# Performance work log

Hardware: AMD Instinct MI355X
Metric: run time of the kernel (lower is better)

## Reference

```python
import jax, jax.numpy as jnp
import numpy as np

B, NQ, NK = 4, 384, 384
D_EQUI, D_QINV, D_KVINV = 64, 256, 256
D_MSG, D_FF, D_OUT = 64, 128, 64
IN_FEATS = 2 * D_MSG + D_EQUI  # 192


def setup_inputs() -> dict:
    key = jax.random.key(0)
    ks = jax.random.split(key, 12)
    s = lambda k, shp, fan: jax.random.normal(k, shp, jnp.float32) / np.sqrt(fan)
    return {
        "q_equi": jax.random.normal(ks[0], (B, NQ, 3, D_EQUI), jnp.float32),
        "q_inv": jax.random.normal(ks[1], (B, NQ, D_QINV), jnp.float32),
        "k_equi": jax.random.normal(ks[2], (B, NK, 3, D_EQUI), jnp.float32),
        "k_inv": jax.random.normal(ks[3], (B, NK, D_KVINV), jnp.float32),
        "Wq": s(ks[4], (D_QINV, D_MSG), D_QINV),
        "bq": jnp.zeros((D_MSG,), jnp.float32),
        "Wk": s(ks[5], (D_KVINV, D_MSG), D_KVINV),
        "bk": jnp.zeros((D_MSG,), jnp.float32),
        "W1": s(ks[6], (IN_FEATS, D_FF), IN_FEATS),
        "b1": jnp.zeros((D_FF,), jnp.float32),
        "W2": s(ks[7], (D_FF, D_OUT), D_FF),
        "b2": jnp.zeros((D_OUT,), jnp.float32),
    }


def reference(q_equi, q_inv, k_equi, k_inv, Wq, bq, Wk, bk, W1, b1, W2, b2):
    # dotprods over the 3 spatial coords, per equi-channel: [B, Nq, Nk, d_equi]
    dotprods = jnp.einsum("bqcd,bkcd->bqkd", q_equi, k_equi)
    q_msg = q_inv @ Wq + bq  # [B, Nq, d_msg]
    k_msg = k_inv @ Wk + bk  # [B, Nk, d_msg]
    b, nq, dm = q_msg.shape
    nk = k_msg.shape[1]
    # expand + concat -> [B, Nq, Nk, in_feats]
    feats = jnp.concatenate(
        [
            jnp.broadcast_to(q_msg[:, :, None, :], (b, nq, nk, dm)),
            jnp.broadcast_to(k_msg[:, None, :, :], (b, nq, nk, dm)),
            dotprods,
        ],
        axis=-1,
    )
    h = jax.nn.silu(feats @ W1 + b1)  # [B, Nq, Nk, d_ff]
    return h @ W2 + b2  # [B, Nq, Nk, d_out]
```

## Files before the change

kernel.cpp:

```cpp
#include <hip/hip_runtime.h>
#include <hip/hip_bf16.h>
#include <stdint.h>
#include <stddef.h>

#define NQ 384
#define NK 384

typedef __attribute__((ext_vector_type(4))) float float4_;
typedef __attribute__((ext_vector_type(8))) short short8;
typedef __attribute__((ext_vector_type(2))) unsigned int uint2_;

__device__ __forceinline__ short f2bf(float f) {
  union { float f; uint32_t u; } v; v.f = f;
  uint32_t u = v.u;
  uint32_t r = (u + 0x7fffu + ((u >> 16) & 1u)) >> 16;
  return (short)r;
}

__device__ __forceinline__ unsigned int pk2(float lo, float hi) {
  __hip_bfloat162 r = __float22bfloat162_rn(make_float2(lo, hi));
  union { __hip_bfloat162 b; unsigned int u; } u; u.b = r;
  return u.u;
}

__global__ __launch_bounds__(256) void prep0(
    const float* __restrict__ Wq, const float* __restrict__ Wk,
    const float* __restrict__ W1, const float* __restrict__ b1,
    const float* __restrict__ bq, const float* __restrict__ bk,
    const float* __restrict__ W2,
    float* __restrict__ Wqc, float* __restrict__ Wkc,
    float* __restrict__ c1, float* __restrict__ c2,
    short* __restrict__ W1dfrag, short* __restrict__ W2frag)
{
  int bid = blockIdx.x, t = threadIdx.x;
  if (bid < 32) {
    int side = bid >> 4;
    int r0 = (bid & 15) * 16;
    const float* W = side ? Wk : Wq;
    const float* W1s = W1 + side * 64 * 128;
    float* Wc = side ? Wkc : Wqc;
    __shared__ float sW[16][64];
    for (int j = t; j < 1024; j += 256) sW[j >> 6][j & 63] = W[(r0 + (j >> 6)) * 64 + (j & 63)];
    __syncthreads();
    int c = t & 127, rg = (t >> 7) * 8;
    float acc[8] = {0.f, 0.f, 0.f, 0.f, 0.f, 0.f, 0.f, 0.f};
    for (int k = 0; k < 64; ++k) {
      float wv = W1s[k * 128 + c];
      #pragma unroll
      for (int j = 0; j < 8; ++j) acc[j] += sW[rg + j][k] * wv;
    }
    for (int j = 0; j < 8; ++j) Wc[(r0 + rg + j) * 128 + c] = acc[j];
  } else if (bid == 32) {
    if (t < 256) {
      int c = t & 127, side = t >> 7;
      const float* bias = side ? bk : bq;
      const float* W1s = W1 + side * 64 * 128;
      float acc = side ? 0.f : b1[c];
      for (int k = 0; k < 64; ++k) acc += bias[k] * W1s[k * 128 + c];
      (side ? c2 : c1)[c] = acc;
    }
  } else {
    for (int idx = t; idx < 8192; idx += 256) {
      int fi = idx >> 9;
      int l  = (idx >> 3) & 63;
      int i  = idx & 7;
      { int n = fi >> 1, s = fi & 1;
        int d = s * 32 + ((l >> 4) << 3) + i;
        int f = n * 16 + (l & 15);
        W1dfrag[idx] = f2bf(W1[(128 + d) * 128 + f]); }
      { int n2 = fi >> 2, s2 = fi & 3;
        int k = s2 * 32 + ((l >> 4) << 3) + i;
        int o = n2 * 16 + (l & 15);
        W2frag[idx] = f2bf(W2[k * 64 + o]); }
    }
  }
}

__global__ __launch_bounds__(256) void prep1(
    const float* __restrict__ q_inv, const float* __restrict__ k_inv,
    const float* __restrict__ Wqc, const float* __restrict__ Wkc,
    const float* __restrict__ c1, const float* __restrict__ c2,
    float* __restrict__ A1, float* __restrict__ A2)
{
  int bid = blockIdx.x, t = threadIdx.x;
  int row0 = bid * 8;
  int side = row0 >= 1536;
  int r0 = row0 - side * 1536;
  const float* inv = (side ? k_inv : q_inv) + (size_t)r0 * 256;
  const float* Wc  = side ? Wkc : Wqc;
  const float* cc  = side ? c2 : c1;
  float* A = (side ? A2 : A1) + (size_t)r0 * 128;

  __shared__ float sI[8][256];
  for (int j = t; j < 2048; j += 256) sI[j >> 8][j & 255] = inv[j];
  __syncthreads();

  int c = t & 127, rg = (t >> 7) * 4;
  float acc[4] = {0.f, 0.f, 0.f, 0.f};
  for (int k = 0; k < 256; ++k) {
    float wv = Wc[k * 128 + c];
    #pragma unroll
    for (int j = 0; j < 4; ++j) acc[j] += sI[rg + j][k] * wv;
  }
  float cv = cc[c];
  #pragma unroll
  for (int j = 0; j < 4; ++j) A[(size_t)(rg + j) * 128 + c] = acc[j] + cv;
}

__global__ __launch_bounds__(512) void main_kernel(
    const float* __restrict__ q_equi, const float* __restrict__ k_equi,
    const float* __restrict__ A1, const float* __restrict__ A2,
    const short* __restrict__ W1dfrag, const short* __restrict__ W2frag,
    const float* __restrict__ b2, float* __restrict__ out)
{
  int bid = blockIdx.x;
  int b = bid / 576;
  int rem = bid - b * 576;
  int tq = rem / 24, tk = rem - (rem / 24) * 24;
  int q0 = tq * 16, k0 = tk * 16;

  __shared__ __align__(16) char smem[32768];
  float* sK = (float*)smem;

  int tid = threadIdx.x;
  int w = tid >> 6, l = tid & 63;
  int g = l >> 4, r16 = l & 15;

  const float* ksrc = k_equi + ((size_t)(b * NK + k0)) * 192;
  {
    int u = tid;
    int r = u / 48, jj = u - r * 48;
    int j = jj ^ (r & 7);
    __builtin_amdgcn_global_load_lds(ksrc + r * 192 + j * 4, smem + u * 16, 16, 0, 0);
    if (tid < 256) {
      int u2 = tid + 512;
      int r2 = u2 / 48, jj2 = u2 - r2 * 48;
      int j2 = jj2 ^ (r2 & 7);
      __builtin_amdgcn_global_load_lds(ksrc + r2 * 192 + j2 * 4, smem + u2 * 16, 16, 0, 0);
    }
  }
  __syncthreads();

  const float* qrow0 = q_equi + ((size_t)(b * NQ + q0 + 2 * w)) * 192;
  const float* krow = sK + r16 * 48 * 4;
  int x7 = r16 & 7;
  short8 afrag[2][2];
  #pragma unroll
  for (int s = 0; s < 2; ++s) {
    int d0 = s * 32 + g * 8;
    float4_ kva[3], kvb[3];
    #pragma unroll
    for (int c = 0; c < 3; ++c) {
      int j0 = c * 16 + s * 8 + g * 2;
      kva[c] = *(const float4_*)&krow[((j0) ^ x7) * 4];
      kvb[c] = *(const float4_*)&krow[((j0 + 1) ^ x7) * 4];
    }
    #pragma unroll
    for (int m = 0; m < 2; ++m) {
      const float* qrow = qrow0 + m * 192;
      float da[4] = {0.f, 0.f, 0.f, 0.f};
      float db[4] = {0.f, 0.f, 0.f, 0.f};
      #pragma unroll
      for (int c = 0; c < 3; ++c) {
        float4_ qva = *(const float4_*)&qrow[c * 64 + d0];
        float4_ qvb = *(const float4_*)&qrow[c * 64 + d0 + 4];
        #pragma unroll
        for (int i = 0; i < 4; ++i) {
          da[i] += qva[i] * kva[c][i];
          db[i] += qvb[i] * kvb[c][i];
        }
      }
      union { short8 s8; unsigned int u[4]; } au;
      au.u[0] = pk2(da[0], da[1]);
      au.u[1] = pk2(da[2], da[3]);
      au.u[2] = pk2(db[0], db[1]);
      au.u[3] = pk2(db[2], db[3]);
      afrag[m][s] = au.s8;
    }
  }
  __syncthreads();

  const float* A1p = A1 + ((size_t)(b * NQ + q0 + 2 * w)) * 128;
  const float* A2p = A2 + ((size_t)(b * NK + k0)) * 128;
  float4_ acc1[2][8];
  #pragma unroll
  for (int ft = 0; ft < 8; ++ft) {
    float4_ a2v = *(const float4_*)&A2p[r16 * 128 + ft * 16 + g * 4];
    acc1[0][ft] = *(const float4_*)&A1p[ft * 16 + g * 4] + a2v;
    acc1[1][ft] = *(const float4_*)&A1p[128 + ft * 16 + g * 4] + a2v;
  }

  #pragma unroll
  for (int ft = 0; ft < 8; ++ft) {
    #pragma unroll
    for (int s = 0; s < 2; ++s) {
      short8 wf = *(const short8*)&W1dfrag[(((ft * 2 + s) * 64) + l) * 8];
      #pragma unroll
      for (int m = 0; m < 2; ++m)
        acc1[m][ft] = __builtin_amdgcn_mfma_f32_16x16x32_bf16(wf, afrag[m][s], acc1[m][ft], 0, 0, 0);
    }
  }

  char* hbase = smem + w * 4096;
  short8 hb[2][4];
  #pragma unroll
  for (int m = 0; m < 2; ++m) {
    #pragma unroll
    for (int ft = 0; ft < 8; ++ft) {
      float4_ x = acc1[m][ft];
      float y0 = x[0] * __builtin_amdgcn_rcpf(1.f + __expf(-x[0]));
      float y1 = x[1] * __builtin_amdgcn_rcpf(1.f + __expf(-x[1]));
      float y2 = x[2] * __builtin_amdgcn_rcpf(1.f + __expf(-x[2]));
      float y3 = x[3] * __builtin_amdgcn_rcpf(1.f + __expf(-x[3]));
      uint2_ pv;
      pv[0] = pk2(y0, y1);
      pv[1] = pk2(y2, y3);
      int byte = (r16 * 256 + ft * 32 + g * 8) ^ ((r16 & 7) << 4);
      *(uint2_*)(hbase + byte) = pv;
    }
    #pragma unroll
    for (int s2 = 0; s2 < 4; ++s2) {
      int byte = (r16 * 256 + s2 * 64 + g * 16) ^ ((r16 & 7) << 4);
      hb[m][s2] = *(const short8*)(hbase + byte);
    }
  }

  float4_ b2v[4];
  #pragma unroll
  for (int ot = 0; ot < 4; ++ot)
    b2v[ot] = *(const float4_*)&b2[ot * 16 + g * 4];
  float4_ acc2[2][4];
  #pragma unroll
  for (int m = 0; m < 2; ++m)
    #pragma unroll
    for (int ot = 0; ot < 4; ++ot) acc2[m][ot] = b2v[ot];
  #pragma unroll
  for (int s2 = 0; s2 < 4; ++s2) {
    #pragma unroll
    for (int ot = 0; ot < 4; ++ot) {
      short8 wf = *(const short8*)&W2frag[(((ot * 4 + s2) * 64) + l) * 8];
      #pragma unroll
      for (int m = 0; m < 2; ++m)
        acc2[m][ot] = __builtin_amdgcn_mfma_f32_16x16x32_bf16(wf, hb[m][s2], acc2[m][ot], 0, 0, 0);
    }
  }

  #pragma unroll
  for (int m = 0; m < 2; ++m) {
    float* op = out + ((size_t)(b * NQ + q0 + 2 * w + m) * NK + k0 + r16) * 64;
    #pragma unroll
    for (int ot = 0; ot < 4; ++ot)
      *(float4_*)(op + ot * 16 + g * 4) = acc2[m][ot];
  }
}

extern "C" void kernel_launch(void* const* d_in, const int* in_sizes, int n_in,
                              void* d_out, int out_size, void* d_ws, size_t ws_size,
                              hipStream_t stream) {
  (void)in_sizes; (void)n_in; (void)out_size; (void)ws_size;
  const float* q_equi = (const float*)d_in[0];
  const float* q_inv  = (const float*)d_in[1];
  const float* k_equi = (const float*)d_in[2];
  const float* k_inv  = (const float*)d_in[3];
  const float* Wq = (const float*)d_in[4];
  const float* bq = (const float*)d_in[5];
  const float* Wk = (const float*)d_in[6];
  const float* bk = (const float*)d_in[7];
  const float* W1 = (const float*)d_in[8];
  const float* b1 = (const float*)d_in[9];
  const float* W2 = (const float*)d_in[10];
  const float* b2 = (const float*)d_in[11];
  float* out = (float*)d_out;

  char* ws = (char*)d_ws;
  float* A1      = (float*)(ws);
  float* A2      = (float*)(ws + 786432);
  short* W1dfrag = (short*)(ws + 1572864);
  short* W2frag  = (short*)(ws + 1589248);
  float* Wqc     = (float*)(ws + 1605632);
  float* Wkc     = (float*)(ws + 1736704);
  float* c1      = (float*)(ws + 1867776);
  float* c2      = (float*)(ws + 1868288);

  prep0<<<34, 256, 0, stream>>>(Wq, Wk, W1, b1, bq, bk, W2, Wqc, Wkc, c1, c2, W1dfrag, W2frag);
  prep1<<<384, 256, 0, stream>>>(q_inv, k_inv, Wqc, Wkc, c1, c2, A1, A2);
  main_kernel<<<2304, 512, 0, stream>>>(q_equi, k_equi, A1, A2, W1dfrag, W2frag, b2, out);
}
```

Measured before the change: 253.7 us.

## Process three k-tiles per block with double-buffered LDS staging of k_equi

Each block now covers 48 keys instead of 16, looping over three 16-key tiles. The k_equi rows for the next tile are loaded asynchronously into a second LDS buffer while the current tile is computed. This cuts the grid from 2304 to 768 blocks, spreads per-block setup (b2 loads, q-row and A1 reuse) over more work, and hides global-load latency. In exchange, LDS per block grows to 56KB, which may limit how many blocks run on a CU at once, and the smaller grid gives less parallel slack to hide latency.

```diff
diff --git a/kernel.cpp b/kernel.cpp
--- a/kernel.cpp
+++ b/kernel.cpp
@@ -5,6 +5,7 @@
 
 #define NQ 384
 #define NK 384
+#define NKT 3
 
 typedef __attribute__((ext_vector_type(4))) float float4_;
 typedef __attribute__((ext_vector_type(8))) short short8;
@@ -114,143 +115,158 @@
     const float* __restrict__ b2, float* __restrict__ out)
 {
   int bid = blockIdx.x;
-  int b = bid / 576;
-  int rem = bid - b * 576;
-  int tq = rem / 24, tk = rem - (rem / 24) * 24;
-  int q0 = tq * 16, k0 = tk * 16;
-
-  __shared__ __align__(16) char smem[32768];
-  float* sK = (float*)smem;
+  int b = bid / 192;
+  int rem = bid - b * 192;
+  int tq = rem >> 3, tk = rem & 7;
+  int q0 = tq * 16, k0 = tk * 48;
+
+  __shared__ __align__(16) char smem[57344];
 
   int tid = threadIdx.x;
   int w = tid >> 6, l = tid & 63;
   int g = l >> 4, r16 = l & 15;
 
-  const float* ksrc = k_equi + ((size_t)(b * NK + k0)) * 192;
-  {
+  const float* kbase = k_equi + ((size_t)(b * NK + k0)) * 192;
+
+  auto stage = [&](int tt, char* dst) {
+    const float* src = kbase + (size_t)tt * 16 * 192;
     int u = tid;
     int r = u / 48, jj = u - r * 48;
     int j = jj ^ (r & 7);
-    __builtin_amdgcn_global_load_lds(ksrc + r * 192 + j * 4, smem + u * 16, 16, 0, 0);
+    __builtin_amdgcn_global_load_lds(src + r * 192 + j * 4, dst + u * 16, 16, 0, 0);
     if (tid < 256) {
       int u2 = tid + 512;
       int r2 = u2 / 48, jj2 = u2 - r2 * 48;
       int j2 = jj2 ^ (r2 & 7);
-      __builtin_amdgcn_global_load_lds(ksrc + r2 * 192 + j2 * 4, smem + u2 * 16, 16, 0, 0);
-    }
-  }
-  __syncthreads();
+      __builtin_amdgcn_global_load_lds(src + r2 * 192 + j2 * 4, dst + u2 * 16, 16, 0, 0);
+    }
+  };
+
+  stage(0, smem);
 
   const float* qrow0 = q_equi + ((size_t)(b * NQ + q0 + 2 * w)) * 192;
-  const float* krow = sK + r16 * 48 * 4;
-  int x7 = r16 & 7;
-  short8 afrag[2][2];
-  #pragma unroll
-  for (int s = 0; s < 2; ++s) {
-    int d0 = s * 32 + g * 8;
-    float4_ kva[3], kvb[3];
-    #pragma unroll
-    for (int c = 0; c < 3; ++c) {
-      int j0 = c * 16 + s * 8 + g * 2;
-      kva[c] = *(const float4_*)&krow[((j0) ^ x7) * 4];
-      kvb[c] = *(const float4_*)&krow[((j0 + 1) ^ x7) * 4];
-    }
-    #pragma unroll
-    for (int m = 0; m < 2; ++m) {
-      const float* qrow = qrow0 + m * 192;
-      float da[4] = {0.f, 0.f, 0.f, 0.f};
-      float db[4] = {0.f, 0.f, 0.f, 0.f};
-      #pragma unroll
-      for (int c = 0; c < 3; ++c) {
-        float4_ qva = *(const float4_*)&qrow[c * 64 + d0];
-        float4_ qvb = *(const float4_*)&qrow[c * 64 + d0 + 4];
-        #pragma unroll
-        for (int i = 0; i < 4; ++i) {
-          da[i] += qva[i] * kva[c][i];
-          db[i] += qvb[i] * kvb[c][i];
-        }
-      }
-      union { short8 s8; unsigned int u[4]; } au;
-      au.u[0] = pk2(da[0], da[1]);
-      au.u[1] = pk2(da[2], da[3]);
-      au.u[2] = pk2(db[0], db[1]);
-      au.u[3] = pk2(db[2], db[3]);
-      afrag[m][s] = au.s8;
-    }
-  }
-  __syncthreads();
-
   const float* A1p = A1 + ((size_t)(b * NQ + q0 + 2 * w)) * 128;
   const float* A2p = A2 + ((size_t)(b * NK + k0)) * 128;
-  float4_ acc1[2][8];
-  #pragma unroll
-  for (int ft = 0; ft < 8; ++ft) {
-    float4_ a2v = *(const float4_*)&A2p[r16 * 128 + ft * 16 + g * 4];
-    acc1[0][ft] = *(const float4_*)&A1p[ft * 16 + g * 4] + a2v;
-    acc1[1][ft] = *(const float4_*)&A1p[128 + ft * 16 + g * 4] + a2v;
-  }
-
-  #pragma unroll
-  for (int ft = 0; ft < 8; ++ft) {
-    #pragma unroll
-    for (int s = 0; s < 2; ++s) {
-      short8 wf = *(const short8*)&W1dfrag[(((ft * 2 + s) * 64) + l) * 8];
-      #pragma unroll
-      for (int m = 0; m < 2; ++m)
-        acc1[m][ft] = __builtin_amdgcn_mfma_f32_16x16x32_bf16(wf, afrag[m][s], acc1[m][ft], 0, 0, 0);
-    }
-  }
-
-  char* hbase = smem + w * 4096;
-  short8 hb[2][4];
-  #pragma unroll
-  for (int m = 0; m < 2; ++m) {
-    #pragma unroll
-    for (int ft = 0; ft < 8; ++ft) {
-      float4_ x = acc1[m][ft];
-      float y0 = x[0] * __builtin_amdgcn_rcpf(1.f + __expf(-x[0]));
-      float y1 = x[1] * __builtin_amdgcn_rcpf(1.f + __expf(-x[1]));
-      float y2 = x[2] * __builtin_amdgcn_rcpf(1.f + __expf(-x[2]));
-      float y3 = x[3] * __builtin_amdgcn_rcpf(1.f + __expf(-x[3]));
-      uint2_ pv;
-      pv[0] = pk2(y0, y1);
-      pv[1] = pk2(y2, y3);
-      int byte = (r16 * 256 + ft * 32 + g * 8) ^ ((r16 & 7) << 4);
-      *(uint2_*)(hbase + byte) = pv;
-    }
-    #pragma unroll
-    for (int s2 = 0; s2 < 4; ++s2) {
-      int byte = (r16 * 256 + s2 * 64 + g * 16) ^ ((r16 & 7) << 4);
-      hb[m][s2] = *(const short8*)(hbase + byte);
-    }
-  }
+  char* hbase = smem + 24576 + w * 4096;
+  int x7 = r16 & 7;
 
   float4_ b2v[4];
   #pragma unroll
   for (int ot = 0; ot < 4; ++ot)
     b2v[ot] = *(const float4_*)&b2[ot * 16 + g * 4];
-  float4_ acc2[2][4];
-  #pragma unroll
-  for (int m = 0; m < 2; ++m)
-    #pragma unroll
-    for (int ot = 0; ot < 4; ++ot) acc2[m][ot] = b2v[ot];
-  #pragma unroll
-  for (int s2 = 0; s2 < 4; ++s2) {
-    #pragma unroll
-    for (int ot = 0; ot < 4; ++ot) {
-      short8 wf = *(const short8*)&W2frag[(((ot * 4 + s2) * 64) + l) * 8];
-      #pragma unroll
-      for (int m = 0; m < 2; ++m)
-        acc2[m][ot] = __builtin_amdgcn_mfma_f32_16x16x32_bf16(wf, hb[m][s2], acc2[m][ot], 0, 0, 0);
-    }
-  }
-
-  #pragma unroll
-  for (int m = 0; m < 2; ++m) {
-    float* op = out + ((size_t)(b * NQ + q0 + 2 * w + m) * NK + k0 + r16) * 64;
-    #pragma unroll
-    for (int ot = 0; ot < 4; ++ot)
-      *(float4_*)(op + ot * 16 + g * 4) = acc2[m][ot];
+
+  __syncthreads();
+
+  #pragma unroll 1
+  for (int t = 0; t < NKT; ++t) {
+    char* cur = smem + (t & 1) * 12288;
+
+    if (t < NKT - 1) stage(t + 1, smem + ((t + 1) & 1) * 12288);
+
+    const float* krow = (const float*)cur + r16 * 192;
+    short8 afrag[2][2];
+    #pragma unroll
+    for (int s = 0; s < 2; ++s) {
+      int d0 = s * 32 + g * 8;
+      float4_ kva[3], kvb[3];
+      #pragma unroll
+      for (int c = 0; c < 3; ++c) {
+        int j0 = c * 16 + s * 8 + g * 2;
+        kva[c] = *(const float4_*)&krow[((j0) ^ x7) * 4];
+        kvb[c] = *(const float4_*)&krow[((j0 + 1) ^ x7) * 4];
+      }
+      #pragma unroll
+      for (int m = 0; m < 2; ++m) {
+        const float* qrow = qrow0 + m * 192;
+        float da[4] = {0.f, 0.f, 0.f, 0.f};
+        float db[4] = {0.f, 0.f, 0.f, 0.f};
+        #pragma unroll
+        for (int c = 0; c < 3; ++c) {
+          float4_ qva = *(const float4_*)&qrow[c * 64 + d0];
+          float4_ qvb = *(const float4_*)&qrow[c * 64 + d0 + 4];
+          #pragma unroll
+          for (int i = 0; i < 4; ++i) {
+            da[i] += qva[i] * kva[c][i];
+            db[i] += qvb[i] * kvb[c][i];
+          }
+        }
+        union { short8 s8; unsigned int u[4]; } au;
+        au.u[0] = pk2(da[0], da[1]);
+        au.u[1] = pk2(da[2], da[3]);
+        au.u[2] = pk2(db[0], db[1]);
+        au.u[3] = pk2(db[2], db[3]);
+        afrag[m][s] = au.s8;
+      }
+    }
+
+    if (t < NKT - 1) __syncthreads();
+
+    const float* A2t = A2p + (size_t)t * 16 * 128;
+    float4_ acc1[2][8];
+    #pragma unroll
+    for (int ft = 0; ft < 8; ++ft) {
+      float4_ a2v = *(const float4_*)&A2t[r16 * 128 + ft * 16 + g * 4];
+      acc1[0][ft] = *(const float4_*)&A1p[ft * 16 + g * 4] + a2v;
+      acc1[1][ft] = *(const float4_*)&A1p[128 + ft * 16 + g * 4] + a2v;
+    }
+
+    #pragma unroll
+    for (int ft = 0; ft < 8; ++ft) {
+      #pragma unroll
+      for (int s = 0; s < 2; ++s) {
+        short8 wf = *(const short8*)&W1dfrag[(((ft * 2 + s) * 64) + l) * 8];
+        #pragma unroll
+        for (int m = 0; m < 2; ++m)
+          acc1[m][ft] = __builtin_amdgcn_mfma_f32_16x16x32_bf16(wf, afrag[m][s], acc1[m][ft], 0, 0, 0);
+      }
+    }
+
+    short8 hb[2][4];
+    #pragma unroll
+    for (int m = 0; m < 2; ++m) {
+      #pragma unroll
+      for (int ft = 0; ft < 8; ++ft) {
+        float4_ x = acc1[m][ft];
+        float y0 = x[0] * __builtin_amdgcn_rcpf(1.f + __expf(-x[0]));
+        float y1 = x[1] * __builtin_amdgcn_rcpf(1.f + __expf(-x[1]));
+        float y2 = x[2] * __builtin_amdgcn_rcpf(1.f + __expf(-x[2]));
+        float y3 = x[3] * __builtin_amdgcn_rcpf(1.f + __expf(-x[3]));
+        uint2_ pv;
+        pv[0] = pk2(y0, y1);
+        pv[1] = pk2(y2, y3);
+        int byte = (r16 * 256 + ft * 32 + g * 8) ^ ((r16 & 7) << 4);
+        *(uint2_*)(hbase + byte) = pv;
+      }
+      #pragma unroll
+      for (int s2 = 0; s2 < 4; ++s2) {
+        int byte = (r16 * 256 + s2 * 64 + g * 16) ^ ((r16 & 7) << 4);
+        hb[m][s2] = *(const short8*)(hbase + byte);
+      }
+    }
+
+    float4_ acc2[2][4];
+    #pragma unroll
+    for (int m = 0; m < 2; ++m)
+      #pragma unroll
+      for (int ot = 0; ot < 4; ++ot) acc2[m][ot] = b2v[ot];
+    #pragma unroll
+    for (int s2 = 0; s2 < 4; ++s2) {
+      #pragma unroll
+      for (int ot = 0; ot < 4; ++ot) {
+        short8 wf = *(const short8*)&W2frag[(((ot * 4 + s2) * 64) + l) * 8];
+        #pragma unroll
+        for (int m = 0; m < 2; ++m)
+          acc2[m][ot] = __builtin_amdgcn_mfma_f32_16x16x32_bf16(wf, hb[m][s2], acc2[m][ot], 0, 0, 0);
+      }
+    }
+
+    #pragma unroll
+    for (int m = 0; m < 2; ++m) {
+      float* op = out + ((size_t)(b * NQ + q0 + 2 * w + m) * NK + k0 + t * 16 + r16) * 64;
+      #pragma unroll
+      for (int ot = 0; ot < 4; ++ot)
+        *(float4_*)(op + ot * 16 + g * 4) = acc2[m][ot];
+    }
   }
 }
 
@@ -284,5 +300,5 @@
 
   prep0<<<34, 256, 0, stream>>>(Wq, Wk, W1, b1, bq, bk, W2, Wqc, Wkc, c1, c2, W1dfrag, W2frag);
   prep1<<<384, 256, 0, stream>>>(q_inv, k_inv, Wqc, Wkc, c1, c2, A1, A2);
-  main_kernel<<<2304, 512, 0, stream>>>(q_equi, k_equi, A1, A2, W1dfrag, W2frag, b2, out);
-}
+  main_kernel<<<768, 512, 0, stream>>>(q_equi, k_equi, A1, A2, W1dfrag, W2frag, b2, out);
+}
```

Result: slower. 422.5 us (+66.5%).
